# Optimization experiments

Hardware: AMD Instinct MI355X
Metric: run time of the kernel (lower is better)

## Reference

```python
import jax, jax.numpy as jnp
import numpy as np


def setup_inputs() -> dict:
    key = jax.random.key(0)
    k1, k2, k3, k4 = jax.random.split(key, 4)
    B, S, T = 512, 512, 128
    emissions = jax.random.normal(k1, (B, S, T), dtype=jnp.float32)
    tags = jax.random.randint(k2, (B, S), 0, T, dtype=jnp.int64)
    mask = jax.random.randint(k3, (B, S), 0, 2, dtype=jnp.int32).astype(jnp.bool_)
    transitions = jax.random.normal(k4, (T, T), dtype=jnp.float32)
    return {"emissions": emissions, "tags": tags, "mask": mask, "transitions": transitions}


def reference(emissions, tags, mask, transitions):
    # emissions: [B, S, T], tags: [B, S] int, mask: [B, S] bool, transitions: [T, T]
    m = mask.astype(emissions.dtype)  # [B, S]
    # emission score: sum_b,t mask[b,t] * emissions[b,t,tags[b,t]]
    emit = jnp.take_along_axis(emissions, tags[..., None], axis=-1)[..., 0]  # [B, S]
    emit_score = jnp.sum(emit * m)
    # transition score: for t>0 where mask[b,t] and mask[b,t-1]
    pair_m = m[:, 1:] * m[:, :-1]  # [B, S-1]
    trans = transitions[tags[:, :-1], tags[:, 1:]]  # [B, S-1]
    trans_score = jnp.sum(trans * pair_m)
    return (emit_score + trans_score) / jnp.sum(m)
```

## Files before the change

kernel.cpp:

```cpp
#include <hip/hip_runtime.h>


constexpr int S = 512;
constexpr int T = 128;
constexpr int TOTAL = 512 * 512;
constexpr int NBLK = TOTAL / (256 * 2);

__global__ __launch_bounds__(256) void crf_partial_kernel(
        const float* __restrict__ emissions,
        const int* __restrict__ tags,
        const int* __restrict__ mask,
        const float* __restrict__ transitions,
        double* __restrict__ part_val,
        unsigned int* __restrict__ part_cnt) {
    int gid = blockIdx.x * 256 + threadIdx.x;
    int idx = gid << 1;

    int2 tg = ((const int2*)tags)[gid];
    int2 mk = ((const int2*)mask)[gid];

    float contrib = 0.0f;
    unsigned int cnt = 0;

    if (mk.x) { contrib += emissions[((size_t)idx << 7) + (size_t)tg.x]; ++cnt; }
    if (mk.y) { contrib += emissions[(((size_t)idx + 1) << 7) + (size_t)tg.y]; ++cnt; }

    if (mk.x & mk.y) contrib += transitions[(tg.x << 7) + tg.y];

    int s0 = idx & (S - 1);
    if (s0 != S - 2) {
        if (mk.y) {
            int m2 = mask[idx + 2];
            if (m2) contrib += transitions[(tg.y << 7) + tags[idx + 2]];
        }
    }

    double val = (double)contrib;
    #pragma unroll
    for (int off = 32; off > 0; off >>= 1) {
        val += __shfl_down(val, off, 64);
        cnt += __shfl_down(cnt, off, 64);
    }

    __shared__ double s_val[4];
    __shared__ unsigned int s_cnt[4];
    int wave = threadIdx.x >> 6;
    int lane = threadIdx.x & 63;
    if (lane == 0) { s_val[wave] = val; s_cnt[wave] = cnt; }
    __syncthreads();

    if (threadIdx.x == 0) {
        part_val[blockIdx.x] = s_val[0] + s_val[1] + s_val[2] + s_val[3];
        part_cnt[blockIdx.x] = s_cnt[0] + s_cnt[1] + s_cnt[2] + s_cnt[3];
    }
}

__global__ __launch_bounds__(256) void crf_final_kernel(
        const double* __restrict__ part_val,
        const unsigned int* __restrict__ part_cnt,
        float* __restrict__ out) {
    double v = 0.0;
    unsigned int c = 0;
    #pragma unroll
    for (int i = 0; i < NBLK / 256; ++i) {
        int j = threadIdx.x + i * 256;
        v += part_val[j];
        c += part_cnt[j];
    }
    #pragma unroll
    for (int off = 32; off > 0; off >>= 1) {
        v += __shfl_down(v, off, 64);
        c += __shfl_down(c, off, 64);
    }
    __shared__ double s_val[4];
    __shared__ unsigned int s_cnt[4];
    int wave = threadIdx.x >> 6;
    int lane = threadIdx.x & 63;
    if (lane == 0) { s_val[wave] = v; s_cnt[wave] = c; }
    __syncthreads();
    if (threadIdx.x == 0) {
        double vv = s_val[0] + s_val[1] + s_val[2] + s_val[3];
        unsigned int cc = s_cnt[0] + s_cnt[1] + s_cnt[2] + s_cnt[3];
        out[0] = (float)(vv / (double)cc);
    }
}

extern "C" void kernel_launch(void* const* d_in, const int* in_sizes, int n_in,
                              void* d_out, int out_size, void* d_ws, size_t ws_size,
                              hipStream_t stream) {
    const float* emissions   = (const float*)d_in[0];
    const int*   tags        = (const int*)d_in[1];
    const int*   mask        = (const int*)d_in[2];
    const float* transitions = (const float*)d_in[3];
    float* out = (float*)d_out;

    double*       part_val = (double*)d_ws;
    unsigned int* part_cnt = (unsigned int*)((char*)d_ws + NBLK * sizeof(double));

    crf_partial_kernel<<<NBLK, 256, 0, stream>>>(emissions, tags, mask, transitions,
                                                 part_val, part_cnt);
    crf_final_kernel<<<1, 256, 0, stream>>>(part_val, part_cnt, out);
}
```

Measured before the change: 11.35 us.

## Fuse final reduction into partial kernel via per-block release/acquire flags

```diff
diff --git a/kernel.cpp b/kernel.cpp
--- a/kernel.cpp
+++ b/kernel.cpp
@@ -2,17 +2,18 @@
 
 
 constexpr int S = 512;
-constexpr int T = 128;
 constexpr int TOTAL = 512 * 512;
 constexpr int NBLK = TOTAL / (256 * 2);
 
-__global__ __launch_bounds__(256) void crf_partial_kernel(
+__global__ __launch_bounds__(256) void crf_fused_kernel(
         const float* __restrict__ emissions,
         const int* __restrict__ tags,
         const int* __restrict__ mask,
         const float* __restrict__ transitions,
         double* __restrict__ part_val,
-        unsigned int* __restrict__ part_cnt) {
+        unsigned int* __restrict__ part_cnt,
+        unsigned int* __restrict__ flags,
+        float* __restrict__ out) {
     int gid = blockIdx.x * 256 + threadIdx.x;
     int idx = gid << 1;
 
@@ -28,11 +29,8 @@
     if (mk.x & mk.y) contrib += transitions[(tg.x << 7) + tg.y];
 
     int s0 = idx & (S - 1);
-    if (s0 != S - 2) {
-        if (mk.y) {
-            int m2 = mask[idx + 2];
-            if (m2) contrib += transitions[(tg.y << 7) + tags[idx + 2]];
-        }
+    if (s0 != S - 2 && mk.y) {
+        if (mask[idx + 2]) contrib += transitions[(tg.y << 7) + tags[idx + 2]];
     }
 
     double val = (double)contrib;
@@ -52,36 +50,39 @@
     if (threadIdx.x == 0) {
         part_val[blockIdx.x] = s_val[0] + s_val[1] + s_val[2] + s_val[3];
         part_cnt[blockIdx.x] = s_cnt[0] + s_cnt[1] + s_cnt[2] + s_cnt[3];
+        __hip_atomic_store(&flags[blockIdx.x], 1u, __ATOMIC_RELEASE,
+                           __HIP_MEMORY_SCOPE_AGENT);
     }
-}
 
-__global__ __launch_bounds__(256) void crf_final_kernel(
-        const double* __restrict__ part_val,
-        const unsigned int* __restrict__ part_cnt,
-        float* __restrict__ out) {
-    double v = 0.0;
-    unsigned int c = 0;
-    #pragma unroll
-    for (int i = 0; i < NBLK / 256; ++i) {
-        int j = threadIdx.x + i * 256;
-        v += part_val[j];
-        c += part_cnt[j];
-    }
-    #pragma unroll
-    for (int off = 32; off > 0; off >>= 1) {
-        v += __shfl_down(v, off, 64);
-        c += __shfl_down(c, off, 64);
-    }
-    __shared__ double s_val[4];
-    __shared__ unsigned int s_cnt[4];
-    int wave = threadIdx.x >> 6;
-    int lane = threadIdx.x & 63;
-    if (lane == 0) { s_val[wave] = v; s_cnt[wave] = c; }
-    __syncthreads();
-    if (threadIdx.x == 0) {
-        double vv = s_val[0] + s_val[1] + s_val[2] + s_val[3];
-        unsigned int cc = s_cnt[0] + s_cnt[1] + s_cnt[2] + s_cnt[3];
-        out[0] = (float)(vv / (double)cc);
+    if (blockIdx.x == 0) {
+        int t = threadIdx.x;
+        double v = 0.0;
+        unsigned int c = 0;
+        #pragma unroll
+        for (int i = 0; i < NBLK / 256; ++i) {
+            int j = t + i * 256;
+            while (__hip_atomic_load(&flags[j], __ATOMIC_ACQUIRE,
+                                     __HIP_MEMORY_SCOPE_AGENT) != 1u) { }
+            v += part_val[j];
+            c += part_cnt[j];
+            __hip_atomic_store(&flags[j], 0u, __ATOMIC_RELAXED,
+                               __HIP_MEMORY_SCOPE_AGENT);
+        }
+
+        #pragma unroll
+        for (int off = 32; off > 0; off >>= 1) {
+            v += __shfl_down(v, off, 64);
+            c += __shfl_down(c, off, 64);
+        }
+        __shared__ double f_val[4];
+        __shared__ unsigned int f_cnt[4];
+        if (lane == 0) { f_val[wave] = v; f_cnt[wave] = c; }
+        __syncthreads();
+        if (t == 0) {
+            double vv = f_val[0] + f_val[1] + f_val[2] + f_val[3];
+            unsigned int cc = f_cnt[0] + f_cnt[1] + f_cnt[2] + f_cnt[3];
+            out[0] = (float)(vv / (double)cc);
+        }
     }
 }
 
@@ -96,8 +97,8 @@
 
     double*       part_val = (double*)d_ws;
     unsigned int* part_cnt = (unsigned int*)((char*)d_ws + NBLK * sizeof(double));
+    unsigned int* flags    = (unsigned int*)((char*)d_ws + NBLK * (sizeof(double) + sizeof(unsigned int)));
 
-    crf_partial_kernel<<<NBLK, 256, 0, stream>>>(emissions, tags, mask, transitions,
-                                                 part_val, part_cnt);
-    crf_final_kernel<<<1, 256, 0, stream>>>(part_val, part_cnt, out);
+    crf_fused_kernel<<<NBLK, 256, 0, stream>>>(emissions, tags, mask, transitions,
+                                               part_val, part_cnt, flags, out);
 }
```

Result: slower. 14.59 us (+28.5%).
